# Kernel optimization log

Hardware: AMD Instinct MI355X
Metric: run time of the kernel (lower is better)

## Reference

```python
import jax, jax.numpy as jnp
import numpy as np

LN_EPS = 1e-5

def layernorm(x, w, b):
    mu = jnp.mean(x, axis=-1, keepdims=True)
    var = jnp.mean(jnp.square(x - mu), axis=-1, keepdims=True)
    return (x - mu) * jax.lax.rsqrt(var + LN_EPS) * w + b

def l2_normalize(x, eps=1e-12):
    n = jnp.sqrt(jnp.sum(jnp.square(x), axis=-1, keepdims=True))
    return x / jnp.maximum(n, eps)

def setup_inputs() -> dict:
    key = jax.random.key(0)
    k1, k2 = jax.random.split(key)
    B, D, Npix = 8, 64, 32768
    K, P = 19, 5
    return {
        "base_feature": jax.random.normal(k1, (B, D, Npix), dtype=jnp.float32),
        "means": jax.random.normal(k2, (K, P, D), dtype=jnp.float32) * 0.02,  # trunc_normal_(std=0.02)
        "diagonal": jnp.ones((K, P, D), dtype=jnp.float32),
        "feat_w": jnp.ones((D,), dtype=jnp.float32),
        "feat_b": jnp.zeros((D,), dtype=jnp.float32),
        "mask_w": jnp.ones((K,), dtype=jnp.float32),
        "mask_b": jnp.zeros((K,), dtype=jnp.float32),
    }

def gmm_log_prob(x, mu, scale):
    # x: [N, D]; mu, scale: [KP, D]  (MultivariateNormalDiag with scale_diag=scale)
    # log p = -0.5 * sum(((x-mu)/s)^2) - sum(log s) - 0.5*D*log(2*pi)
    D = x.shape[-1]
    inv2 = 1.0 / jnp.square(scale)                      # [KP, D]
    quad = (jnp.square(x) @ inv2.T                       # [N, KP]
            - 2.0 * (x @ (mu * inv2).T)
            + jnp.sum(jnp.square(mu) * inv2, axis=-1))
    log_norm = jnp.sum(jnp.log(scale), axis=-1) + 0.5 * D * jnp.log(2.0 * jnp.pi)
    return -0.5 * quad - log_norm                        # [N, KP]

def reference(base_feature, means, diagonal, feat_w, feat_b, mask_w, mask_b):
    B, D, Npix = base_feature.shape
    K, P, _ = means.shape
    # 'b c n -> (b n) c'
    _c = jnp.transpose(base_feature, (0, 2, 1)).reshape(B * Npix, D)
    _c = layernorm(_c, feat_w, feat_b)
    _c = l2_normalize(_c)
    means_n = l2_normalize(means)                        # means.data.copy_(l2_normalize(means))
    logp = gmm_log_prob(_c, means_n.reshape(K * P, D), diagonal.reshape(K * P, D))
    final_probs = logp.reshape(-1, K, P)                 # [(b n), K, P]
    _m_prob = jnp.max(final_probs, axis=-1)              # amax over components -> [(b n), K]
    out_seg = layernorm(_m_prob, mask_w, mask_b)         # mask_norm
    # '(b n) k -> b k n'
    out_seg = jnp.transpose(out_seg.reshape(B, Npix, K), (0, 2, 1))
    return out_seg
```

## Files before the change

### kernel.cpp

```cpp
#include <hip/hip_runtime.h>
#include <math.h>

#define BB    8
#define DD    64
#define NPIX  32768
#define KK    19
#define PP    5
#define NROW  112

#define XDW    2048
#define CSTOFF 8192

typedef _Float16 half8  __attribute__((ext_vector_type(8)));
typedef __fp16   half2t __attribute__((ext_vector_type(2)));
typedef float    f32x4  __attribute__((ext_vector_type(4)));

union H8 { half8 v; half2t p[4]; };

__device__ __forceinline__ void gload16(const void* g, void* l) {
    __builtin_amdgcn_global_load_lds(
        (const __attribute__((address_space(1))) void*)g,
        (__attribute__((address_space(3))) void*)l, 16, 0, 0);
}

__global__ __launch_bounds__(64) void gmm_prep(
        const float* __restrict__ means, const float* __restrict__ diag,
        const float* __restrict__ feat_w, const float* __restrict__ feat_b,
        _Float16* __restrict__ Ch, float* __restrict__ cst,
        float* __restrict__ scal) {
    const int R = blockIdx.x;
    const int d = threadIdx.x;
    if (R == NROW) {
        float w = feat_w[d], b = feat_b[d];
        float s0 = w * w, s1 = w * b, s2 = b * b;
        #pragma unroll
        for (int off = 32; off; off >>= 1) {
            s0 += __shfl_xor(s0, off);
            s1 += __shfl_xor(s1, off);
            s2 += __shfl_xor(s2, off);
        }
        if (d == 0) { scal[0] = s0; scal[1] = s1; scal[2] = s2; }
        return;
    }
    int g, p; bool valid;
    if (R < 80)      { g = 4 * (R >> 4) + ((R >> 2) & 3); p = R & 3; valid = (g < KK); }
    else if (R < 96) { g = 4 * ((R - 80) & 3) + ((R - 80) >> 2); p = 4; valid = true; }
    else             { g = 16 + ((R - 96) >> 2); p = 4; valid = ((R & 3) == 0) && (g < KK); }
    if (valid) {
        const int j = 5 * g + p;
        float mu = means[j * DD + d];
        float sc = diag[j * DD + d];
        float ss = mu * mu;
        #pragma unroll
        for (int off = 32; off; off >>= 1) ss += __shfl_xor(ss, off);
        float inv = 1.f / fmaxf(sqrtf(ss), 1e-12f);
        float mn = mu * inv;
        float i2 = 1.f / (sc * sc);
        Ch[R * 128 + 2 * d]     = (_Float16)(mn * i2);
        Ch[R * 128 + 2 * d + 1] = (_Float16)(-0.5f * i2);
        float c1 = mn * mn * i2;
        float c2 = logf(sc);
        #pragma unroll
        for (int off = 32; off; off >>= 1) {
            c1 += __shfl_xor(c1, off);
            c2 += __shfl_xor(c2, off);
        }
        if (d == 0) cst[R] = -0.5f * c1 - c2;
    } else {
        Ch[R * 128 + 2 * d]     = (_Float16)0.f;
        Ch[R * 128 + 2 * d + 1] = (_Float16)0.f;
        if (d == 0) cst[R] = 0.f;
    }
}

__global__ __launch_bounds__(256, 3) void gmm_main(
        const float* __restrict__ bf,
        const float* __restrict__ feat_w, const float* __restrict__ feat_b,
        const float* __restrict__ mask_w, const float* __restrict__ mask_b,
        const _Float16* __restrict__ Ch, const float* __restrict__ cst,
        const float* __restrict__ scal, float* __restrict__ out) {
    __shared__ __align__(16) float smem[8304];

    const int tid  = threadIdx.x;
    const int w    = tid >> 6;
    const int lane = tid & 63;
    const int m15  = lane & 15;
    const int q    = lane >> 4;
    const int bidx = blockIdx.x;
    const int b    = bidx >> 8;
    const int n0   = ((bidx & 255) << 7) + (w << 5);
    float* lp = smem + w * XDW;

    const int rr  = lane >> 3;
    const int c4s = ((lane & 7) * 4) ^ (rr << 2);
    const float* xgb = bf + (size_t)b * (DD * NPIX) + n0;
    #pragma unroll
    for (int j = 0; j < 8; ++j)
        gload16(xgb + (size_t)(8 * j + rr) * NPIX + c4s, lp + 8 * j * 32);

    if (tid < NROW) smem[CSTOFF + tid] = cst[tid];

    float4 wv[4], bv[4];
    #pragma unroll
    for (int ks = 0; ks < 4; ++ks) {
        wv[ks] = *(const float4*)(feat_w + ks * 16 + q * 4);
        bv[ks] = *(const float4*)(feat_b + ks * 16 + q * 4);
    }
    const float W2 = scal[0], WB = scal[1], B2 = scal[2];

    __syncthreads();

    float xs0[16], xs1[16];
    #pragma unroll
    for (int ks = 0; ks < 4; ++ks)
        #pragma unroll
        for (int i = 0; i < 4; ++i) {
            const int row = 16 * ks + 4 * q + i;
            const int sw  = (row & 7) << 2;
            xs0[ks * 4 + i] = lp[row * 32 + (m15 ^ sw)];
            xs1[ks * 4 + i] = lp[row * 32 + ((m15 + 16) ^ sw)];
        }

    __syncthreads();

    {
        const char* Cg = (const char*)Ch;
        #pragma unroll
        for (int i = 0; i < 7; ++i) {
            const int f   = (w * 7 + i) * 64 + lane;
            const int row = f >> 4, ch = f & 15;
            gload16(Cg + (size_t)row * 256 + ((ch ^ (row & 15)) * 16),
                    smem + (size_t)(w * 7 + i) * 256);
        }
    }

    float S1a = 0.f, S2a = 0.f, S3a = 0.f, S4a = 0.f, S5a = 0.f;
    float S1b = 0.f, S2b = 0.f, S3b = 0.f, S4b = 0.f, S5b = 0.f;
    #pragma unroll
    for (int ks = 0; ks < 4; ++ks)
        #pragma unroll
        for (int i = 0; i < 4; ++i) {
            float wd = ((const float*)&wv[ks])[i];
            float bd = ((const float*)&bv[ks])[i];
            float xa = xs0[ks * 4 + i], xb = xs1[ks * 4 + i];
            float ta = wd * xa, tb = wd * xb;
            S1a += xa; S2a = fmaf(xa, xa, S2a); S3a = fmaf(ta, ta, S3a);
            S4a = fmaf(ta, wd, S4a); S5a = fmaf(ta, bd, S5a);
            S1b += xb; S2b = fmaf(xb, xb, S2b); S3b = fmaf(tb, tb, S3b);
            S4b = fmaf(tb, wd, S4b); S5b = fmaf(tb, bd, S5b);
        }
    S1a += __shfl_xor(S1a, 16); S1a += __shfl_xor(S1a, 32);
    S2a += __shfl_xor(S2a, 16); S2a += __shfl_xor(S2a, 32);
    S3a += __shfl_xor(S3a, 16); S3a += __shfl_xor(S3a, 32);
    S4a += __shfl_xor(S4a, 16); S4a += __shfl_xor(S4a, 32);
    S5a += __shfl_xor(S5a, 16); S5a += __shfl_xor(S5a, 32);
    S1b += __shfl_xor(S1b, 16); S1b += __shfl_xor(S1b, 32);
    S2b += __shfl_xor(S2b, 16); S2b += __shfl_xor(S2b, 32);
    S3b += __shfl_xor(S3b, 16); S3b += __shfl_xor(S3b, 32);
    S4b += __shfl_xor(S4b, 16); S4b += __shfl_xor(S4b, 32);
    S5b += __shfl_xor(S5b, 16); S5b += __shfl_xor(S5b, 32);

    float al0, e0, f0, al1, e1, f1;
    {
        float mu  = S1a * (1.f / 64.f);
        float var = fmaxf(S2a * (1.f / 64.f) - mu * mu, 0.f);
        float r   = rsqrtf(var + 1e-5f);
        float Sy2 = r * r * (S3a - 2.f * mu * S4a + mu * mu * W2)
                  + 2.f * r * (S5a - mu * WB) + B2;
        float invn = 1.f / fmaxf(sqrtf(fmaxf(Sy2, 0.f)), 1e-12f);
        al0 = invn * r; e0 = invn; f0 = -al0 * mu;
    }
    {
        float mu  = S1b * (1.f / 64.f);
        float var = fmaxf(S2b * (1.f / 64.f) - mu * mu, 0.f);
        float r   = rsqrtf(var + 1e-5f);
        float Sy2 = r * r * (S3b - 2.f * mu * S4b + mu * mu * W2)
                  + 2.f * r * (S5b - mu * WB) + B2;
        float invn = 1.f / fmaxf(sqrtf(fmaxf(Sy2, 0.f)), 1e-12f);
        al1 = invn * r; e1 = invn; f1 = -al1 * mu;
    }

    H8 Uh[2][4], Ul[2][4];
    #pragma unroll
    for (int ks = 0; ks < 4; ++ks) {
        #pragma unroll
        for (int i = 0; i < 4; ++i) {
            float wd = ((const float*)&wv[ks])[i];
            float bd = ((const float*)&bv[ks])[i];
            float c0 = fmaf(f0, wd, e0 * bd);
            float c1 = fmaf(f1, wd, e1 * bd);
            float u0 = fmaf(al0, wd * xs0[ks * 4 + i], c0);
            float u1 = fmaf(al1, wd * xs1[ks * 4 + i], c1);
            float q0 = u0 * u0, q1 = u1 * u1;
            half2t h0 = __builtin_amdgcn_cvt_pkrtz(u0, q0);
            half2t h1 = __builtin_amdgcn_cvt_pkrtz(u1, q1);
            half2t l0 = __builtin_amdgcn_cvt_pkrtz(u0 - (float)h0[0], q0 - (float)h0[1]);
            half2t l1 = __builtin_amdgcn_cvt_pkrtz(u1 - (float)h1[0], q1 - (float)h1[1]);
            Uh[0][ks].p[i] = h0; Ul[0][ks].p[i] = l0;
            Uh[1][ks].p[i] = h1; Ul[1][ks].p[i] = l1;
        }
    }

    __syncthreads();

    float m0[5], m1[5];
    #pragma unroll
    for (int t = 0; t < 7; ++t) {
        half8 Ac[4];
        #pragma unroll
        for (int ks = 0; ks < 4; ++ks)
            Ac[ks] = *(const half8*)((const char*)smem
                        + (size_t)(16 * t + m15) * 256 + (((ks * 4 + q) ^ m15) * 16));
        const float4 cv = *(const float4*)(smem + CSTOFF + 16 * t + 4 * q);
        f32x4 a0 = {0.f, 0.f, 0.f, 0.f}, a1 = {0.f, 0.f, 0.f, 0.f};
        #pragma unroll
        for (int ks = 0; ks < 4; ++ks) {
            a0 = __builtin_amdgcn_mfma_f32_16x16x32_f16(Ac[ks], Uh[0][ks].v, a0, 0, 0, 0);
            a1 = __builtin_amdgcn_mfma_f32_16x16x32_f16(Ac[ks], Uh[1][ks].v, a1, 0, 0, 0);
        }
        #pragma unroll
        for (int ks = 0; ks < 4; ++ks) {
            a0 = __builtin_amdgcn_mfma_f32_16x16x32_f16(Ac[ks], Ul[0][ks].v, a0, 0, 0, 0);
            a1 = __builtin_amdgcn_mfma_f32_16x16x32_f16(Ac[ks], Ul[1][ks].v, a1, 0, 0, 0);
        }
        if (t < 5) {
            m0[t] = fmaxf(fmaxf(a0[0] + cv.x, a0[1] + cv.y), fmaxf(a0[2] + cv.z, a0[3] + cv.w));
            m1[t] = fmaxf(fmaxf(a1[0] + cv.x, a1[1] + cv.y), fmaxf(a1[2] + cv.z, a1[3] + cv.w));
        } else if (t == 5) {
            m0[0] = fmaxf(m0[0], a0[0] + cv.x);
            m0[1] = fmaxf(m0[1], a0[1] + cv.y);
            m0[2] = fmaxf(m0[2], a0[2] + cv.z);
            m0[3] = fmaxf(m0[3], a0[3] + cv.w);
            m1[0] = fmaxf(m1[0], a1[0] + cv.x);
            m1[1] = fmaxf(m1[1], a1[1] + cv.y);
            m1[2] = fmaxf(m1[2], a1[2] + cv.z);
            m1[3] = fmaxf(m1[3], a1[3] + cv.w);
        } else {
            m0[4] = fmaxf(m0[4], a0[0] + cv.x);
            m1[4] = fmaxf(m1[4], a1[0] + cv.x);
        }
    }

    const bool v4 = (q < 3);
    float S0 = m0[0] + m0[1] + m0[2] + m0[3] + (v4 ? m0[4] : 0.f);
    float S1 = m1[0] + m1[1] + m1[2] + m1[3] + (v4 ? m1[4] : 0.f);
    S0 += __shfl_xor(S0, 16); S0 += __shfl_xor(S0, 32);
    S1 += __shfl_xor(S1, 16); S1 += __shfl_xor(S1, 32);
    const float mu0 = S0 * (1.f / 19.f), mu1 = S1 * (1.f / 19.f);
    float V0, V1;
    {
        float d0 = m0[0] - mu0, d1 = m0[1] - mu0, d2 = m0[2] - mu0;
        float d3 = m0[3] - mu0, d4 = m0[4] - mu0;
        V0 = d0 * d0 + d1 * d1 + d2 * d2 + d3 * d3 + (v4 ? d4 * d4 : 0.f);
    }
    {
        float d0 = m1[0] - mu1, d1 = m1[1] - mu1, d2 = m1[2] - mu1;
        float d3 = m1[3] - mu1, d4 = m1[4] - mu1;
        V1 = d0 * d0 + d1 * d1 + d2 * d2 + d3 * d3 + (v4 ? d4 * d4 : 0.f);
    }
    V0 += __shfl_xor(V0, 16); V0 += __shfl_xor(V0, 32);
    V1 += __shfl_xor(V1, 16); V1 += __shfl_xor(V1, 32);
    const float r0 = rsqrtf(V0 * (1.f / 19.f) + 1e-5f);
    const float r1 = rsqrtf(V1 * (1.f / 19.f) + 1e-5f);

    __syncthreads();

    #pragma unroll
    for (int t = 0; t < 5; ++t) {
        const int k = 4 * t + q;
        if (t < 4 || v4) {
            const float mw = mask_w[k], mb = mask_b[k];
            lp[k * 32 + m15]      = (m0[t] - mu0) * r0 * mw + mb;
            lp[k * 32 + 16 + m15] = (m1[t] - mu1) * r1 * mw + mb;
        }
    }

    __syncthreads();

    float* ob = out + (size_t)b * (KK * NPIX) + n0;
    #pragma unroll
    for (int rnd = 0; rnd < 3; ++rnd) {
        const int idx = rnd * 64 + lane;
        if (idx < 152) {
            const int k = idx >> 3, cc = (idx & 7) * 4;
            float4 v = *(const float4*)(lp + k * 32 + cc);
            *(float4*)(ob + (size_t)k * NPIX + cc) = v;
        }
    }
}

extern "C" void kernel_launch(void* const* d_in, const int* in_sizes, int n_in,
                              void* d_out, int out_size, void* d_ws, size_t ws_size,
                              hipStream_t stream) {
    const float* base_feature = (const float*)d_in[0];
    const float* means        = (const float*)d_in[1];
    const float* diagonal     = (const float*)d_in[2];
    const float* feat_w       = (const float*)d_in[3];
    const float* feat_b       = (const float*)d_in[4];
    const float* mask_w       = (const float*)d_in[5];
    const float* mask_b       = (const float*)d_in[6];
    float* out = (float*)d_out;

    _Float16* Ch = (_Float16*)d_ws;
    float* cst   = (float*)(Ch + NROW * 128);
    float* scal  = cst + NROW;

    gmm_prep<<<NROW + 1, 64, 0, stream>>>(means, diagonal, feat_w, feat_b, Ch, cst, scal);

    gmm_main<<<(BB * NPIX) / 128, 256, 0, stream>>>(
        base_feature, feat_w, feat_b, mask_w, mask_b, Ch, cst, scal, out);
}
```

Measured before the change: 122.4 us.

## Make blocks persistent over four pixel tiles with register-prefetched next tile

Each block now handles 512 pixels in four chunks instead of 128. The GMM coefficient table is staged into LDS once per block instead of once per 128 pixels. The next chunk's input is prefetched into registers while the current chunk's MFMA work runs, then written to LDS after a barrier. Separate LDS regions for input and output, plus sched_barrier-fenced syncs, keep the chunks from aliasing. In exchange, occupancy drops to 2 blocks per CU, the grid shrinks to 512 blocks, and register pressure rises from the prefetch buffers.

```diff
diff --git a/kernel.cpp b/kernel.cpp
--- a/kernel.cpp
+++ b/kernel.cpp
@@ -8,8 +8,9 @@
 #define PP    5
 #define NROW  112
 
-#define XDW    2048
-#define CSTOFF 8192
+#define CSTL  7168
+#define XB    7296
+#define OBASE 15488
 
 typedef _Float16 half8  __attribute__((ext_vector_type(8)));
 typedef __fp16   half2t __attribute__((ext_vector_type(2)));
@@ -21,6 +22,12 @@
     __builtin_amdgcn_global_load_lds(
         (const __attribute__((address_space(1))) void*)g,
         (__attribute__((address_space(3))) void*)l, 16, 0, 0);
+}
+
+__device__ __forceinline__ void barrier_fenced() {
+    __builtin_amdgcn_sched_barrier(0);
+    __syncthreads();
+    __builtin_amdgcn_sched_barrier(0);
 }
 
 __global__ __launch_bounds__(64) void gmm_prep(
@@ -73,13 +80,13 @@
     }
 }
 
-__global__ __launch_bounds__(256, 3) void gmm_main(
+__global__ __launch_bounds__(256, 2) void gmm_main(
         const float* __restrict__ bf,
         const float* __restrict__ feat_w, const float* __restrict__ feat_b,
         const float* __restrict__ mask_w, const float* __restrict__ mask_b,
         const _Float16* __restrict__ Ch, const float* __restrict__ cst,
         const float* __restrict__ scal, float* __restrict__ out) {
-    __shared__ __align__(16) float smem[8304];
+    __shared__ __align__(16) float smem[17920];
 
     const int tid  = threadIdx.x;
     const int w    = tid >> 6;
@@ -87,18 +94,31 @@
     const int m15  = lane & 15;
     const int q    = lane >> 4;
     const int bidx = blockIdx.x;
-    const int b    = bidx >> 8;
-    const int n0   = ((bidx & 255) << 7) + (w << 5);
-    float* lp = smem + w * XDW;
+    const int b    = bidx >> 6;
+    const int nb   = (bidx & 63) << 9;
+    float* xp = smem + XB + w * 2048;
+    float* op = smem + OBASE + w * 608;
 
     const int rr  = lane >> 3;
-    const int c4s = ((lane & 7) * 4) ^ (rr << 2);
-    const float* xgb = bf + (size_t)b * (DD * NPIX) + n0;
-    #pragma unroll
-    for (int j = 0; j < 8; ++j)
-        gload16(xgb + (size_t)(8 * j + rr) * NPIX + c4s, lp + 8 * j * 32);
-
-    if (tid < NROW) smem[CSTOFF + tid] = cst[tid];
+    const int c4  = (lane & 7) * 4;
+    const int c4s = c4 ^ (rr << 2);
+    const float* xim = bf + (size_t)b * (DD * NPIX);
+
+    {
+        const float* xg0 = xim + nb + (w << 5);
+        #pragma unroll
+        for (int j = 0; j < 8; ++j)
+            gload16(xg0 + (size_t)(8 * j + rr) * NPIX + c4s, xp + 8 * j * 32);
+        const char* Cg = (const char*)Ch;
+        #pragma unroll
+        for (int i = 0; i < 7; ++i) {
+            const int f   = (w * 7 + i) * 64 + lane;
+            const int row = f >> 4, ch = f & 15;
+            gload16(Cg + (size_t)row * 256 + ((ch ^ (row & 15)) * 16),
+                    smem + (size_t)(w * 7 + i) * 256);
+        }
+        if (tid < NROW) smem[CSTL + tid] = cst[tid];
+    }
 
     float4 wv[4], bv[4];
     #pragma unroll
@@ -107,184 +127,186 @@
         bv[ks] = *(const float4*)(feat_b + ks * 16 + q * 4);
     }
     const float W2 = scal[0], WB = scal[1], B2 = scal[2];
-
-    __syncthreads();
-
-    float xs0[16], xs1[16];
+    const bool v4 = (q < 3);
+
+    barrier_fenced();
+
     #pragma unroll
-    for (int ks = 0; ks < 4; ++ks)
-        #pragma unroll
-        for (int i = 0; i < 4; ++i) {
-            const int row = 16 * ks + 4 * q + i;
-            const int sw  = (row & 7) << 2;
-            xs0[ks * 4 + i] = lp[row * 32 + (m15 ^ sw)];
-            xs1[ks * 4 + i] = lp[row * 32 + ((m15 + 16) ^ sw)];
-        }
-
-    __syncthreads();
-
-    {
-        const char* Cg = (const char*)Ch;
-        #pragma unroll
-        for (int i = 0; i < 7; ++i) {
-            const int f   = (w * 7 + i) * 64 + lane;
-            const int row = f >> 4, ch = f & 15;
-            gload16(Cg + (size_t)row * 256 + ((ch ^ (row & 15)) * 16),
-                    smem + (size_t)(w * 7 + i) * 256);
-        }
-    }
-
-    float S1a = 0.f, S2a = 0.f, S3a = 0.f, S4a = 0.f, S5a = 0.f;
-    float S1b = 0.f, S2b = 0.f, S3b = 0.f, S4b = 0.f, S5b = 0.f;
-    #pragma unroll
-    for (int ks = 0; ks < 4; ++ks)
-        #pragma unroll
-        for (int i = 0; i < 4; ++i) {
-            float wd = ((const float*)&wv[ks])[i];
-            float bd = ((const float*)&bv[ks])[i];
-            float xa = xs0[ks * 4 + i], xb = xs1[ks * 4 + i];
-            float ta = wd * xa, tb = wd * xb;
-            S1a += xa; S2a = fmaf(xa, xa, S2a); S3a = fmaf(ta, ta, S3a);
-            S4a = fmaf(ta, wd, S4a); S5a = fmaf(ta, bd, S5a);
-            S1b += xb; S2b = fmaf(xb, xb, S2b); S3b = fmaf(tb, tb, S3b);
-            S4b = fmaf(tb, wd, S4b); S5b = fmaf(tb, bd, S5b);
-        }
-    S1a += __shfl_xor(S1a, 16); S1a += __shfl_xor(S1a, 32);
-    S2a += __shfl_xor(S2a, 16); S2a += __shfl_xor(S2a, 32);
-    S3a += __shfl_xor(S3a, 16); S3a += __shfl_xor(S3a, 32);
-    S4a += __shfl_xor(S4a, 16); S4a += __shfl_xor(S4a, 32);
-    S5a += __shfl_xor(S5a, 16); S5a += __shfl_xor(S5a, 32);
-    S1b += __shfl_xor(S1b, 16); S1b += __shfl_xor(S1b, 32);
-    S2b += __shfl_xor(S2b, 16); S2b += __shfl_xor(S2b, 32);
-    S3b += __shfl_xor(S3b, 16); S3b += __shfl_xor(S3b, 32);
-    S4b += __shfl_xor(S4b, 16); S4b += __shfl_xor(S4b, 32);
-    S5b += __shfl_xor(S5b, 16); S5b += __shfl_xor(S5b, 32);
-
-    float al0, e0, f0, al1, e1, f1;
-    {
-        float mu  = S1a * (1.f / 64.f);
-        float var = fmaxf(S2a * (1.f / 64.f) - mu * mu, 0.f);
-        float r   = rsqrtf(var + 1e-5f);
-        float Sy2 = r * r * (S3a - 2.f * mu * S4a + mu * mu * W2)
-                  + 2.f * r * (S5a - mu * WB) + B2;
-        float invn = 1.f / fmaxf(sqrtf(fmaxf(Sy2, 0.f)), 1e-12f);
-        al0 = invn * r; e0 = invn; f0 = -al0 * mu;
-    }
-    {
-        float mu  = S1b * (1.f / 64.f);
-        float var = fmaxf(S2b * (1.f / 64.f) - mu * mu, 0.f);
-        float r   = rsqrtf(var + 1e-5f);
-        float Sy2 = r * r * (S3b - 2.f * mu * S4b + mu * mu * W2)
-                  + 2.f * r * (S5b - mu * WB) + B2;
-        float invn = 1.f / fmaxf(sqrtf(fmaxf(Sy2, 0.f)), 1e-12f);
-        al1 = invn * r; e1 = invn; f1 = -al1 * mu;
-    }
-
-    H8 Uh[2][4], Ul[2][4];
-    #pragma unroll
-    for (int ks = 0; ks < 4; ++ks) {
-        #pragma unroll
-        for (int i = 0; i < 4; ++i) {
-            float wd = ((const float*)&wv[ks])[i];
-            float bd = ((const float*)&bv[ks])[i];
-            float c0 = fmaf(f0, wd, e0 * bd);
-            float c1 = fmaf(f1, wd, e1 * bd);
-            float u0 = fmaf(al0, wd * xs0[ks * 4 + i], c0);
-            float u1 = fmaf(al1, wd * xs1[ks * 4 + i], c1);
-            float q0 = u0 * u0, q1 = u1 * u1;
-            half2t h0 = __builtin_amdgcn_cvt_pkrtz(u0, q0);
-            half2t h1 = __builtin_amdgcn_cvt_pkrtz(u1, q1);
-            half2t l0 = __builtin_amdgcn_cvt_pkrtz(u0 - (float)h0[0], q0 - (float)h0[1]);
-            half2t l1 = __builtin_amdgcn_cvt_pkrtz(u1 - (float)h1[0], q1 - (float)h1[1]);
-            Uh[0][ks].p[i] = h0; Ul[0][ks].p[i] = l0;
-            Uh[1][ks].p[i] = h1; Ul[1][ks].p[i] = l1;
-        }
-    }
-
-    __syncthreads();
-
-    float m0[5], m1[5];
-    #pragma unroll
-    for (int t = 0; t < 7; ++t) {
-        half8 Ac[4];
+    for (int c = 0; c < 4; ++c) {
+        float4 xv[8];
+        if (c < 3) {
+            const float* xg1 = xim + nb + ((c + 1) << 7) + (w << 5);
+            #pragma unroll
+            for (int j = 0; j < 8; ++j)
+                xv[j] = *(const float4*)(xg1 + (size_t)(8 * j + rr) * NPIX + c4);
+        }
+
+        float xs0[16], xs1[16];
         #pragma unroll
         for (int ks = 0; ks < 4; ++ks)
-            Ac[ks] = *(const half8*)((const char*)smem
-                        + (size_t)(16 * t + m15) * 256 + (((ks * 4 + q) ^ m15) * 16));
-        const float4 cv = *(const float4*)(smem + CSTOFF + 16 * t + 4 * q);
-        f32x4 a0 = {0.f, 0.f, 0.f, 0.f}, a1 = {0.f, 0.f, 0.f, 0.f};
+            #pragma unroll
+            for (int i = 0; i < 4; ++i) {
+                const int row = 16 * ks + 4 * q + i;
+                const int sw  = (row & 7) << 2;
+                xs0[ks * 4 + i] = xp[row * 32 + (m15 ^ sw)];
+                xs1[ks * 4 + i] = xp[row * 32 + ((m15 + 16) ^ sw)];
+            }
+
+        float S1a = 0.f, S2a = 0.f, S3a = 0.f, S4a = 0.f, S5a = 0.f;
+        float S1b = 0.f, S2b = 0.f, S3b = 0.f, S4b = 0.f, S5b = 0.f;
+        #pragma unroll
+        for (int ks = 0; ks < 4; ++ks)
+            #pragma unroll
+            for (int i = 0; i < 4; ++i) {
+                float wd = ((const float*)&wv[ks])[i];
+                float bd = ((const float*)&bv[ks])[i];
+                float xa = xs0[ks * 4 + i], xb = xs1[ks * 4 + i];
+                float ta = wd * xa, tb = wd * xb;
+                S1a += xa; S2a = fmaf(xa, xa, S2a); S3a = fmaf(ta, ta, S3a);
+                S4a = fmaf(ta, wd, S4a); S5a = fmaf(ta, bd, S5a);
+                S1b += xb; S2b = fmaf(xb, xb, S2b); S3b = fmaf(tb, tb, S3b);
+                S4b = fmaf(tb, wd, S4b); S5b = fmaf(tb, bd, S5b);
+            }
+        S1a += __shfl_xor(S1a, 16); S1a += __shfl_xor(S1a, 32);
+        S2a += __shfl_xor(S2a, 16); S2a += __shfl_xor(S2a, 32);
+        S3a += __shfl_xor(S3a, 16); S3a += __shfl_xor(S3a, 32);
+        S4a += __shfl_xor(S4a, 16); S4a += __shfl_xor(S4a, 32);
+        S5a += __shfl_xor(S5a, 16); S5a += __shfl_xor(S5a, 32);
+        S1b += __shfl_xor(S1b, 16); S1b += __shfl_xor(S1b, 32);
+        S2b += __shfl_xor(S2b, 16); S2b += __shfl_xor(S2b, 32);
+        S3b += __shfl_xor(S3b, 16); S3b += __shfl_xor(S3b, 32);
+        S4b += __shfl_xor(S4b, 16); S4b += __shfl_xor(S4b, 32);
+        S5b += __shfl_xor(S5b, 16); S5b += __shfl_xor(S5b, 32);
+
+        float al0, e0, f0, al1, e1, f1;
+        {
+            float mu  = S1a * (1.f / 64.f);
+            float var = fmaxf(S2a * (1.f / 64.f) - mu * mu, 0.f);
+            float r   = rsqrtf(var + 1e-5f);
+            float Sy2 = r * r * (S3a - 2.f * mu * S4a + mu * mu * W2)
+                      + 2.f * r * (S5a - mu * WB) + B2;
+            float invn = 1.f / fmaxf(sqrtf(fmaxf(Sy2, 0.f)), 1e-12f);
+            al0 = invn * r; e0 = invn; f0 = -al0 * mu;
+        }
+        {
+            float mu  = S1b * (1.f / 64.f);
+            float var = fmaxf(S2b * (1.f / 64.f) - mu * mu, 0.f);
+            float r   = rsqrtf(var + 1e-5f);
+            float Sy2 = r * r * (S3b - 2.f * mu * S4b + mu * mu * W2)
+                      + 2.f * r * (S5b - mu * WB) + B2;
+            float invn = 1.f / fmaxf(sqrtf(fmaxf(Sy2, 0.f)), 1e-12f);
+            al1 = invn * r; e1 = invn; f1 = -al1 * mu;
+        }
+
+        H8 Uh[2][4], Ul[2][4];
         #pragma unroll
         for (int ks = 0; ks < 4; ++ks) {
-            a0 = __builtin_amdgcn_mfma_f32_16x16x32_f16(Ac[ks], Uh[0][ks].v, a0, 0, 0, 0);
-            a1 = __builtin_amdgcn_mfma_f32_16x16x32_f16(Ac[ks], Uh[1][ks].v, a1, 0, 0, 0);
-        }
-        #pragma unroll
-        for (int ks = 0; ks < 4; ++ks) {
-            a0 = __builtin_amdgcn_mfma_f32_16x16x32_f16(Ac[ks], Ul[0][ks].v, a0, 0, 0, 0);
-            a1 = __builtin_amdgcn_mfma_f32_16x16x32_f16(Ac[ks], Ul[1][ks].v, a1, 0, 0, 0);
-        }
-        if (t < 5) {
-            m0[t] = fmaxf(fmaxf(a0[0] + cv.x, a0[1] + cv.y), fmaxf(a0[2] + cv.z, a0[3] + cv.w));
-            m1[t] = fmaxf(fmaxf(a1[0] + cv.x, a1[1] + cv.y), fmaxf(a1[2] + cv.z, a1[3] + cv.w));
-        } else if (t == 5) {
-            m0[0] = fmaxf(m0[0], a0[0] + cv.x);
-            m0[1] = fmaxf(m0[1], a0[1] + cv.y);
-            m0[2] = fmaxf(m0[2], a0[2] + cv.z);
-            m0[3] = fmaxf(m0[3], a0[3] + cv.w);
-            m1[0] = fmaxf(m1[0], a1[0] + cv.x);
-            m1[1] = fmaxf(m1[1], a1[1] + cv.y);
-            m1[2] = fmaxf(m1[2], a1[2] + cv.z);
-            m1[3] = fmaxf(m1[3], a1[3] + cv.w);
-        } else {
-            m0[4] = fmaxf(m0[4], a0[0] + cv.x);
-            m1[4] = fmaxf(m1[4], a1[0] + cv.x);
-        }
-    }
-
-    const bool v4 = (q < 3);
-    float S0 = m0[0] + m0[1] + m0[2] + m0[3] + (v4 ? m0[4] : 0.f);
-    float S1 = m1[0] + m1[1] + m1[2] + m1[3] + (v4 ? m1[4] : 0.f);
-    S0 += __shfl_xor(S0, 16); S0 += __shfl_xor(S0, 32);
-    S1 += __shfl_xor(S1, 16); S1 += __shfl_xor(S1, 32);
-    const float mu0 = S0 * (1.f / 19.f), mu1 = S1 * (1.f / 19.f);
-    float V0, V1;
-    {
-        float d0 = m0[0] - mu0, d1 = m0[1] - mu0, d2 = m0[2] - mu0;
-        float d3 = m0[3] - mu0, d4 = m0[4] - mu0;
-        V0 = d0 * d0 + d1 * d1 + d2 * d2 + d3 * d3 + (v4 ? d4 * d4 : 0.f);
-    }
-    {
-        float d0 = m1[0] - mu1, d1 = m1[1] - mu1, d2 = m1[2] - mu1;
-        float d3 = m1[3] - mu1, d4 = m1[4] - mu1;
-        V1 = d0 * d0 + d1 * d1 + d2 * d2 + d3 * d3 + (v4 ? d4 * d4 : 0.f);
-    }
-    V0 += __shfl_xor(V0, 16); V0 += __shfl_xor(V0, 32);
-    V1 += __shfl_xor(V1, 16); V1 += __shfl_xor(V1, 32);
-    const float r0 = rsqrtf(V0 * (1.f / 19.f) + 1e-5f);
-    const float r1 = rsqrtf(V1 * (1.f / 19.f) + 1e-5f);
-
-    __syncthreads();
-
-    #pragma unroll
-    for (int t = 0; t < 5; ++t) {
-        const int k = 4 * t + q;
-        if (t < 4 || v4) {
-            const float mw = mask_w[k], mb = mask_b[k];
-            lp[k * 32 + m15]      = (m0[t] - mu0) * r0 * mw + mb;
-            lp[k * 32 + 16 + m15] = (m1[t] - mu1) * r1 * mw + mb;
-        }
-    }
-
-    __syncthreads();
-
-    float* ob = out + (size_t)b * (KK * NPIX) + n0;
-    #pragma unroll
-    for (int rnd = 0; rnd < 3; ++rnd) {
-        const int idx = rnd * 64 + lane;
-        if (idx < 152) {
-            const int k = idx >> 3, cc = (idx & 7) * 4;
-            float4 v = *(const float4*)(lp + k * 32 + cc);
-            *(float4*)(ob + (size_t)k * NPIX + cc) = v;
+            #pragma unroll
+            for (int i = 0; i < 4; ++i) {
+                float wd = ((const float*)&wv[ks])[i];
+                float bd = ((const float*)&bv[ks])[i];
+                float c0 = fmaf(f0, wd, e0 * bd);
+                float c1 = fmaf(f1, wd, e1 * bd);
+                float u0 = fmaf(al0, wd * xs0[ks * 4 + i], c0);
+                float u1 = fmaf(al1, wd * xs1[ks * 4 + i], c1);
+                float q0 = u0 * u0, q1 = u1 * u1;
+                half2t h0 = __builtin_amdgcn_cvt_pkrtz(u0, q0);
+                half2t h1 = __builtin_amdgcn_cvt_pkrtz(u1, q1);
+                half2t l0 = __builtin_amdgcn_cvt_pkrtz(u0 - (float)h0[0], q0 - (float)h0[1]);
+                half2t l1 = __builtin_amdgcn_cvt_pkrtz(u1 - (float)h1[0], q1 - (float)h1[1]);
+                Uh[0][ks].p[i] = h0; Ul[0][ks].p[i] = l0;
+                Uh[1][ks].p[i] = h1; Ul[1][ks].p[i] = l1;
+            }
+        }
+
+        barrier_fenced();
+
+        if (c < 3) {
+            #pragma unroll
+            for (int j = 0; j < 8; ++j)
+                *(float4*)(xp + (8 * j + rr) * 32 + c4s) = xv[j];
+        }
+
+        float m0[5], m1[5];
+        #pragma unroll
+        for (int t = 0; t < 7; ++t) {
+            half8 Ac[4];
+            #pragma unroll
+            for (int ks = 0; ks < 4; ++ks)
+                Ac[ks] = *(const half8*)((const char*)smem
+                            + (size_t)(16 * t + m15) * 256 + (((ks * 4 + q) ^ m15) * 16));
+            const float4 cv = *(const float4*)(smem + CSTL + 16 * t + 4 * q);
+            f32x4 a0 = {0.f, 0.f, 0.f, 0.f}, a1 = {0.f, 0.f, 0.f, 0.f};
+            #pragma unroll
+            for (int ks = 0; ks < 4; ++ks) {
+                a0 = __builtin_amdgcn_mfma_f32_16x16x32_f16(Ac[ks], Uh[0][ks].v, a0, 0, 0, 0);
+                a1 = __builtin_amdgcn_mfma_f32_16x16x32_f16(Ac[ks], Uh[1][ks].v, a1, 0, 0, 0);
+            }
+            #pragma unroll
+            for (int ks = 0; ks < 4; ++ks) {
+                a0 = __builtin_amdgcn_mfma_f32_16x16x32_f16(Ac[ks], Ul[0][ks].v, a0, 0, 0, 0);
+                a1 = __builtin_amdgcn_mfma_f32_16x16x32_f16(Ac[ks], Ul[1][ks].v, a1, 0, 0, 0);
+            }
+            if (t < 5) {
+                m0[t] = fmaxf(fmaxf(a0[0] + cv.x, a0[1] + cv.y), fmaxf(a0[2] + cv.z, a0[3] + cv.w));
+                m1[t] = fmaxf(fmaxf(a1[0] + cv.x, a1[1] + cv.y), fmaxf(a1[2] + cv.z, a1[3] + cv.w));
+            } else if (t == 5) {
+                m0[0] = fmaxf(m0[0], a0[0] + cv.x);
+                m0[1] = fmaxf(m0[1], a0[1] + cv.y);
+                m0[2] = fmaxf(m0[2], a0[2] + cv.z);
+                m0[3] = fmaxf(m0[3], a0[3] + cv.w);
+                m1[0] = fmaxf(m1[0], a1[0] + cv.x);
+                m1[1] = fmaxf(m1[1], a1[1] + cv.y);
+                m1[2] = fmaxf(m1[2], a1[2] + cv.z);
+                m1[3] = fmaxf(m1[3], a1[3] + cv.w);
+            } else {
+                m0[4] = fmaxf(m0[4], a0[0] + cv.x);
+                m1[4] = fmaxf(m1[4], a1[0] + cv.x);
+            }
+        }
+
+        float S0 = m0[0] + m0[1] + m0[2] + m0[3] + (v4 ? m0[4] : 0.f);
+        float S1 = m1[0] + m1[1] + m1[2] + m1[3] + (v4 ? m1[4] : 0.f);
+        S0 += __shfl_xor(S0, 16); S0 += __shfl_xor(S0, 32);
+        S1 += __shfl_xor(S1, 16); S1 += __shfl_xor(S1, 32);
+        const float mu0 = S0 * (1.f / 19.f), mu1 = S1 * (1.f / 19.f);
+        float V0, V1;
+        {
+            float d0 = m0[0] - mu0, d1 = m0[1] - mu0, d2 = m0[2] - mu0;
+            float d3 = m0[3] - mu0, d4 = m0[4] - mu0;
+            V0 = d0 * d0 + d1 * d1 + d2 * d2 + d3 * d3 + (v4 ? d4 * d4 : 0.f);
+        }
+        {
+            float d0 = m1[0] - mu1, d1 = m1[1] - mu1, d2 = m1[2] - mu1;
+            float d3 = m1[3] - mu1, d4 = m1[4] - mu1;
+            V1 = d0 * d0 + d1 * d1 + d2 * d2 + d3 * d3 + (v4 ? d4 * d4 : 0.f);
+        }
+        V0 += __shfl_xor(V0, 16); V0 += __shfl_xor(V0, 32);
+        V1 += __shfl_xor(V1, 16); V1 += __shfl_xor(V1, 32);
+        const float r0 = rsqrtf(V0 * (1.f / 19.f) + 1e-5f);
+        const float r1 = rsqrtf(V1 * (1.f / 19.f) + 1e-5f);
+
+        #pragma unroll
+        for (int t = 0; t < 5; ++t) {
+            const int k = 4 * t + q;
+            if (t < 4 || v4) {
+                const float mw = mask_w[k], mb = mask_b[k];
+                op[k * 32 + m15]      = (m0[t] - mu0) * r0 * mw + mb;
+                op[k * 32 + 16 + m15] = (m1[t] - mu1) * r1 * mw + mb;
+            }
+        }
+
+        barrier_fenced();
+
+        float* ob = out + (size_t)b * (KK * NPIX) + nb + (c << 7) + (w << 5);
+        #pragma unroll
+        for (int rnd = 0; rnd < 3; ++rnd) {
+            const int idx = rnd * 64 + lane;
+            if (idx < 152) {
+                const int k = idx >> 3, cc = (idx & 7) * 4;
+                float4 v = *(const float4*)(op + k * 32 + cc);
+                *(float4*)(ob + (size_t)k * NPIX + cc) = v;
+            }
         }
     }
 }
@@ -307,6 +329,6 @@
 
     gmm_prep<<<NROW + 1, 64, 0, stream>>>(means, diagonal, feat_w, feat_b, Ch, cst, scal);
 
-    gmm_main<<<(BB * NPIX) / 128, 256, 0, stream>>>(
+    gmm_main<<<(BB * NPIX) / 512, 256, 0, stream>>>(
         base_feature, feat_w, feat_b, mask_w, mask_b, Ch, cst, scal, out);
 }
```

Result: slower. 140.7 us (+14.9%).
